# Kernel tuning notes

Hardware: AMD Instinct MI355X
Metric: run time of the kernel (lower is better)

## Reference

```python
import jax, jax.numpy as jnp
import numpy as np

B, N, IN_F, OUT_F = 32, 1024, 256, 256


def setup_inputs() -> dict:
    key = jax.random.key(0)
    k_adj, k_feat, k_w, k_b = jax.random.split(key, 4)
    adjacency = jax.random.uniform(k_adj, (B, N, N), dtype=jnp.float32)  # [B,N,N]
    features = jax.random.normal(k_feat, (B, N, IN_F), dtype=jnp.float32)  # [B,N,in]
    # 'thomas' init ~ uniform(-1/sqrt(fan_in), 1/sqrt(fan_in)) style; scale is
    # irrelevant to correctness-checking, use scaled normal.
    weight = jax.random.normal(k_w, (IN_F, OUT_F), dtype=jnp.float32) / np.sqrt(IN_F)
    bias = jax.random.normal(k_b, (OUT_F,), dtype=jnp.float32) / np.sqrt(IN_F)
    return {"adjacency": adjacency, "features": features, "weight": weight, "bias": bias}


def reference(adjacency, features, weight, bias) -> jnp.ndarray:
    # support = features @ weight : [B,N,out]
    support = jnp.einsum("bni,io->bno", features, weight)
    # output = bmm(adjacency, support) : [B,N,out]
    output = jnp.einsum("bnm,bmo->bno", adjacency, support)
    return output + bias
```

## Files before the change

### kernel.cpp

```cpp
#include <hip/hip_runtime.h>
#include <hip/hip_bf16.h>


typedef __attribute__((__ext_vector_type__(4))) float  f32x4;
typedef __attribute__((__ext_vector_type__(8))) __bf16 bf16x8;
typedef __attribute__((__ext_vector_type__(4))) __bf16 bf16x4;

#define BM  64
#define BN  256
#define BK  32
#define LDP 40

__global__ __launch_bounds__(256) void k_wt(const float* __restrict__ w,
                                            __bf16* __restrict__ Wt) {
  __shared__ __bf16 T[64][65];
  const int bi = blockIdx.x >> 2;
  const int bj = blockIdx.x & 3;
  const int t  = threadIdx.x;
  const int r  = t >> 2;
  const int q  = t & 3;
  const float* src = w + (size_t)(bi * 64 + r) * 256 + bj * 64 + q * 16;
#pragma unroll
  for (int u = 0; u < 4; ++u) {
    f32x4 v = *(const f32x4*)(src + u * 4);
    T[r][q * 16 + u * 4 + 0] = (__bf16)v[0];
    T[r][q * 16 + u * 4 + 1] = (__bf16)v[1];
    T[r][q * 16 + u * 4 + 2] = (__bf16)v[2];
    T[r][q * 16 + u * 4 + 3] = (__bf16)v[3];
  }
  __syncthreads();
  bf16x8 h0, h1;
#pragma unroll
  for (int u = 0; u < 8; ++u) {
    h0[u] = T[q * 16 + u][r];
    h1[u] = T[q * 16 + 8 + u][r];
  }
  __bf16* dst = Wt + (size_t)(bj * 64 + r) * 256 + bi * 64 + q * 16;
  *(bf16x8*)(dst)     = h0;
  *(bf16x8*)(dst + 8) = h1;
}

template <int KTOT, int LDA, int LDB, bool EPI_ST>
__global__ __launch_bounds__(512, 4) void k_gemm(
    const float* __restrict__ Aall, const __bf16* __restrict__ Bg_all,
    const float* __restrict__ bias, float* __restrict__ Out,
    __bf16* __restrict__ St) {
  __shared__ __bf16 As[2][BM * LDP];
  __shared__ __bf16 Bs[2][BN * LDP];

  const int tid  = threadIdx.x;
  const int lane = tid & 63;
  const int wv   = tid >> 6;
  const int wr   = wv >> 2;
  const int wc   = wv & 3;
  const int l16  = lane & 15;
  const int kch  = (lane >> 4) * 8;

  int lg, b, mtile;
  const float*  A;
  const __bf16* Bg;
  if constexpr (EPI_ST) {
    lg    = blockIdx.x;
    b     = lg >> 4;
    mtile = lg & 15;
    A     = Aall + (size_t)lg * BM * LDA;
    Bg    = Bg_all;
  } else {
    const int h = blockIdx.x;
    lg    = (h & 7) * 64 + (h >> 3);
    b     = lg >> 4;
    mtile = lg & 15;
    A     = Aall + (size_t)b * 1024 * 1024 + (size_t)mtile * BM * LDA;
    Bg    = Bg_all + (size_t)b * 256 * 1024;
  }

  const int ar = tid >> 3;
  const int ac = (tid & 7) * 4;
  const int br = tid >> 1;
  const int bh = (tid & 1) * 16;

  const float*  ap = A  + (size_t)ar * LDA + ac;
  const __bf16* bp = Bg + (size_t)br * LDB + bh;

  f32x4  av0, av1;
  bf16x8 bv0[2], bv1[2];

#define LOAD0(k0)                                   \
  av0    = *(const f32x4*)(ap + (k0));              \
  bv0[0] = *(const bf16x8*)(bp + (k0));             \
  bv0[1] = *(const bf16x8*)(bp + (k0) + 8)
#define LOAD1(k0)                                   \
  av1    = *(const f32x4*)(ap + (k0));              \
  bv1[0] = *(const bf16x8*)(bp + (k0));             \
  bv1[1] = *(const bf16x8*)(bp + (k0) + 8)

  auto cvt_write = [&](const f32x4& av, const bf16x8* bv, int buf) {
    bf16x4 h = {(__bf16)av[0], (__bf16)av[1], (__bf16)av[2], (__bf16)av[3]};
    *(bf16x4*)&As[buf][ar * LDP + ac]      = h;
    *(bf16x8*)&Bs[buf][br * LDP + bh]      = bv[0];
    *(bf16x8*)&Bs[buf][br * LDP + bh + 8]  = bv[1];
  };

  f32x4 acc[2][4];
#pragma unroll
  for (int m = 0; m < 2; ++m)
#pragma unroll
    for (int n = 0; n < 4; ++n) acc[m][n] = (f32x4){0.f, 0.f, 0.f, 0.f};

  auto compute = [&](int buf) {
    bf16x8 af[2], bfv[4];
#pragma unroll
    for (int m = 0; m < 2; ++m)
      af[m] = *(const bf16x8*)&As[buf][(wr * 32 + m * 16 + l16) * LDP + kch];
#pragma unroll
    for (int n = 0; n < 4; ++n)
      bfv[n] = *(const bf16x8*)&Bs[buf][(wc * 64 + n * 16 + l16) * LDP + kch];
#pragma unroll
    for (int m = 0; m < 2; ++m)
#pragma unroll
      for (int n = 0; n < 4; ++n)
        acc[m][n] = __builtin_amdgcn_mfma_f32_16x16x32_bf16(af[m], bfv[n], acc[m][n], 0, 0, 0);
  };

  constexpr int NT = KTOT / BK;
  LOAD0(0);
  LOAD1(BK);
  cvt_write(av0, bv0, 0);
  __syncthreads();

  for (int t = 0; t < NT - 2; t += 2) {
    LOAD0((t + 2) * BK);
    compute(0);
    cvt_write(av1, bv1, 1);
    __syncthreads();
    LOAD1((t + 3) * BK);
    compute(1);
    cvt_write(av0, bv0, 0);
    __syncthreads();
  }
  compute(0);
  cvt_write(av1, bv1, 1);
  __syncthreads();
  compute(1);

#undef LOAD0
#undef LOAD1

  const int rg = (lane >> 4) * 4;
  if constexpr (EPI_ST) {
    const int mbase = mtile * BM;
#pragma unroll
    for (int n = 0; n < 4; ++n) {
      const int col = wc * 64 + n * 16 + l16;
      __bf16* dst = St + ((size_t)b * 256 + col) * 1024 + mbase;
#pragma unroll
      for (int m = 0; m < 2; ++m) {
        const int row = wr * 32 + m * 16 + rg;
        bf16x4 hh = {(__bf16)acc[m][n][0], (__bf16)acc[m][n][1],
                     (__bf16)acc[m][n][2], (__bf16)acc[m][n][3]};
        *(bf16x4*)(dst + row) = hh;
      }
    }
  } else {
    float* ob = Out + ((size_t)b * 1024 + (size_t)mtile * BM) * 256;
#pragma unroll
    for (int n = 0; n < 4; ++n) {
      const int col = wc * 64 + n * 16 + l16;
      const float bvs = bias[col];
#pragma unroll
      for (int m = 0; m < 2; ++m) {
        const int row = wr * 32 + m * 16 + rg;
#pragma unroll
        for (int r2 = 0; r2 < 4; ++r2)
          ob[(size_t)(row + r2) * 256 + col] = acc[m][n][r2] + bvs;
      }
    }
  }
}

extern "C" void kernel_launch(void* const* d_in, const int* in_sizes, int n_in,
                              void* d_out, int out_size, void* d_ws, size_t ws_size,
                              hipStream_t stream) {
  const float* adj  = (const float*)d_in[0];
  const float* feat = (const float*)d_in[1];
  const float* w    = (const float*)d_in[2];
  const float* bias = (const float*)d_in[3];
  float* out = (float*)d_out;

  __bf16* Wt = (__bf16*)d_ws;
  __bf16* St = (__bf16*)((char*)d_ws + 131072);

  k_wt<<<16, 256, 0, stream>>>(w, Wt);
  k_gemm<256, 256, 256, true><<<512, 512, 0, stream>>>(feat, Wt, nullptr, nullptr, St);
  k_gemm<1024, 1024, 1024, false><<<512, 512, 0, stream>>>(adj, St, bias, out, nullptr);
}
```

Baseline: 61.68 us.

## Stage GEMM tiles via direct global-to-LDS loads with blocked B layout

Replaces the register-staged load, convert and LDS-write path with global_load_lds direct transfers. A is kept as fp32 in LDS with an XOR swizzle and converted to bf16 at fragment-read time. The intermediate support and transposed weight are stored in a k-blocked [K/8][N][8] layout so each B tile is a contiguous chunk. The aim is to cut VGPR use and load/convert instruction overhead, and to let the copy overlap compute. In exchange the fp32 A tile doubles LDS size, and bf16 conversion is repeated per wave when fragments are read.

```diff
diff --git a/kernel.cpp b/kernel.cpp
--- a/kernel.cpp
+++ b/kernel.cpp
@@ -6,10 +6,15 @@
 typedef __attribute__((__ext_vector_type__(8))) __bf16 bf16x8;
 typedef __attribute__((__ext_vector_type__(4))) __bf16 bf16x4;
 
-#define BM  64
-#define BN  256
-#define BK  32
-#define LDP 40
+#define BM 64
+#define BN 256
+#define BK 32
+
+__device__ __forceinline__ void gld16(const void* g, void* l) {
+  __builtin_amdgcn_global_load_lds(
+      (const __attribute__((address_space(1))) unsigned int*)g,
+      (__attribute__((address_space(3))) unsigned int*)l, 16, 0, 0);
+}
 
 __global__ __launch_bounds__(256) void k_wt(const float* __restrict__ w,
                                             __bf16* __restrict__ Wt) {
@@ -35,70 +40,54 @@
     h0[u] = T[q * 16 + u][r];
     h1[u] = T[q * 16 + 8 + u][r];
   }
-  __bf16* dst = Wt + (size_t)(bj * 64 + r) * 256 + bi * 64 + q * 16;
-  *(bf16x8*)(dst)     = h0;
-  *(bf16x8*)(dst + 8) = h1;
+  __bf16* d0 = Wt + ((size_t)(bi * 8 + q * 2) * 256 + (bj * 64 + r)) * 8;
+  *(bf16x8*)d0          = h0;
+  *(bf16x8*)(d0 + 2048) = h1;
 }
 
-template <int KTOT, int LDA, int LDB, bool EPI_ST>
+template <int KTOT, int LDA, bool EPI_ST>
 __global__ __launch_bounds__(512, 4) void k_gemm(
     const float* __restrict__ Aall, const __bf16* __restrict__ Bg_all,
     const float* __restrict__ bias, float* __restrict__ Out,
     __bf16* __restrict__ St) {
-  __shared__ __bf16 As[2][BM * LDP];
-  __shared__ __bf16 Bs[2][BN * LDP];
+  __shared__ float  Af[2][BM * BK];
+  __shared__ __bf16 Bf[2][4 * BN * 8];
 
   const int tid  = threadIdx.x;
   const int lane = tid & 63;
-  const int wv   = tid >> 6;
-  const int wr   = wv >> 2;
-  const int wc   = wv & 3;
+  const int wid  = tid >> 6;
+  const int wr   = wid >> 2;
+  const int wc   = wid & 3;
   const int l16  = lane & 15;
-  const int kch  = (lane >> 4) * 8;
+  const int g    = lane >> 4;
 
-  int lg, b, mtile;
-  const float*  A;
-  const __bf16* Bg;
+  int b, mtile;
+  const float*  Ablk;
+  const __bf16* Bblk;
   if constexpr (EPI_ST) {
-    lg    = blockIdx.x;
+    const int lg = blockIdx.x;
     b     = lg >> 4;
     mtile = lg & 15;
-    A     = Aall + (size_t)lg * BM * LDA;
-    Bg    = Bg_all;
+    Ablk  = Aall + (size_t)lg * BM * LDA;
+    Bblk  = Bg_all;
   } else {
-    const int h = blockIdx.x;
-    lg    = (h & 7) * 64 + (h >> 3);
+    const int h  = blockIdx.x;
+    const int lg = (h & 7) * 64 + (h >> 3);
     b     = lg >> 4;
     mtile = lg & 15;
-    A     = Aall + (size_t)b * 1024 * 1024 + (size_t)mtile * BM * LDA;
-    Bg    = Bg_all + (size_t)b * 256 * 1024;
+    Ablk  = Aall + (size_t)b * 1024 * 1024 + (size_t)mtile * BM * LDA;
+    Bblk  = Bg_all + (size_t)b * 262144;
   }
 
-  const int ar = tid >> 3;
-  const int ac = (tid & 7) * 4;
-  const int br = tid >> 1;
-  const int bh = (tid & 1) * 16;
+  const int    ar   = tid >> 3;
+  const float* asrc = Ablk + (size_t)ar * LDA + (((tid & 7) ^ (ar & 7)) << 2);
+  const __bf16* bs0 = Bblk + ((size_t)wid * 128 + lane) * 8;
 
-  const float*  ap = A  + (size_t)ar * LDA + ac;
-  const __bf16* bp = Bg + (size_t)br * LDB + bh;
-
-  f32x4  av0, av1;
-  bf16x8 bv0[2], bv1[2];
-
-#define LOAD0(k0)                                   \
-  av0    = *(const f32x4*)(ap + (k0));              \
-  bv0[0] = *(const bf16x8*)(bp + (k0));             \
-  bv0[1] = *(const bf16x8*)(bp + (k0) + 8)
-#define LOAD1(k0)                                   \
-  av1    = *(const f32x4*)(ap + (k0));              \
-  bv1[0] = *(const bf16x8*)(bp + (k0));             \
-  bv1[1] = *(const bf16x8*)(bp + (k0) + 8)
-
-  auto cvt_write = [&](const f32x4& av, const bf16x8* bv, int buf) {
-    bf16x4 h = {(__bf16)av[0], (__bf16)av[1], (__bf16)av[2], (__bf16)av[3]};
-    *(bf16x4*)&As[buf][ar * LDP + ac]      = h;
-    *(bf16x8*)&Bs[buf][br * LDP + bh]      = bv[0];
-    *(bf16x8*)&Bs[buf][br * LDP + bh + 8]  = bv[1];
+  auto stage = [&](int buf, int k0) {
+    gld16(asrc + k0, &Af[buf][wid * 256]);
+    const __bf16* bt = bs0 + (size_t)(k0 >> 3) * 2048;
+    gld16(bt,       &Bf[buf][wid * 1024]);
+    gld16(bt + 512, &Bf[buf][wid * 1024 + 512]);
   };
 
   f32x4 acc[2][4];
@@ -107,58 +96,56 @@
 #pragma unroll
     for (int n = 0; n < 4; ++n) acc[m][n] = (f32x4){0.f, 0.f, 0.f, 0.f};
 
+  const int h7 = l16 & 7;
   auto compute = [&](int buf) {
-    bf16x8 af[2], bfv[4];
+    bf16x8 af[2], bv[4];
 #pragma unroll
-    for (int m = 0; m < 2; ++m)
-      af[m] = *(const bf16x8*)&As[buf][(wr * 32 + m * 16 + l16) * LDP + kch];
+    for (int m = 0; m < 2; ++m) {
+      const float* base = &Af[buf][(wr * 32 + m * 16 + l16) * BK];
+      f32x4 v0 = *(const f32x4*)(base + (((2 * g)     ^ h7) << 2));
+      f32x4 v1 = *(const f32x4*)(base + (((2 * g + 1) ^ h7) << 2));
+      af[m] = (bf16x8){(__bf16)v0[0], (__bf16)v0[1], (__bf16)v0[2], (__bf16)v0[3],
+                       (__bf16)v1[0], (__bf16)v1[1], (__bf16)v1[2], (__bf16)v1[3]};
+    }
 #pragma unroll
     for (int n = 0; n < 4; ++n)
-      bfv[n] = *(const bf16x8*)&Bs[buf][(wc * 64 + n * 16 + l16) * LDP + kch];
+      bv[n] = *(const bf16x8*)&Bf[buf][(g * 256 + wc * 64 + n * 16 + l16) * 8];
 #pragma unroll
     for (int m = 0; m < 2; ++m)
 #pragma unroll
       for (int n = 0; n < 4; ++n)
-        acc[m][n] = __builtin_amdgcn_mfma_f32_16x16x32_bf16(af[m], bfv[n], acc[m][n], 0, 0, 0);
+        acc[m][n] = __builtin_amdgcn_mfma_f32_16x16x32_bf16(af[m], bv[n], acc[m][n], 0, 0, 0);
   };
 
   constexpr int NT = KTOT / BK;
-  LOAD0(0);
-  LOAD1(BK);
-  cvt_write(av0, bv0, 0);
+  stage(0, 0);
   __syncthreads();
-
   for (int t = 0; t < NT - 2; t += 2) {
-    LOAD0((t + 2) * BK);
+    stage(1, (t + 1) * BK);
     compute(0);
-    cvt_write(av1, bv1, 1);
     __syncthreads();
-    LOAD1((t + 3) * BK);
+    stage(0, (t + 2) * BK);
     compute(1);
-    cvt_write(av0, bv0, 0);
     __syncthreads();
   }
+  stage(1, (NT - 1) * BK);
   compute(0);
-  cvt_write(av1, bv1, 1);
   __syncthreads();
   compute(1);
 
-#undef LOAD0
-#undef LOAD1
-
   const int rg = (lane >> 4) * 4;
   if constexpr (EPI_ST) {
-    const int mbase = mtile * BM;
+    __bf16* Stb = St + (size_t)b * 262144;
 #pragma unroll
     for (int n = 0; n < 4; ++n) {
       const int col = wc * 64 + n * 16 + l16;
-      __bf16* dst = St + ((size_t)b * 256 + col) * 1024 + mbase;
 #pragma unroll
       for (int m = 0; m < 2; ++m) {
-        const int row = wr * 32 + m * 16 + rg;
+        const int gm = mtile * 64 + wr * 32 + m * 16 + rg;
+        __bf16* dst = Stb + ((size_t)(gm >> 3) * 256 + col) * 8 + (gm & 7);
         bf16x4 hh = {(__bf16)acc[m][n][0], (__bf16)acc[m][n][1],
                      (__bf16)acc[m][n][2], (__bf16)acc[m][n][3]};
-        *(bf16x4*)(dst + row) = hh;
+        *(bf16x4*)dst = hh;
       }
     }
   } else {
@@ -191,6 +178,6 @@
   __bf16* St = (__bf16*)((char*)d_ws + 131072);
 
   k_wt<<<16, 256, 0, stream>>>(w, Wt);
-  k_gemm<256, 256, 256, true><<<512, 512, 0, stream>>>(feat, Wt, nullptr, nullptr, St);
-  k_gemm<1024, 1024, 1024, false><<<512, 512, 0, stream>>>(adj, St, bias, out, nullptr);
+  k_gemm<256, 256, true><<<512, 512, 0, stream>>>(feat, Wt, nullptr, nullptr, St);
+  k_gemm<1024, 1024, false><<<512, 512, 0, stream>>>(adj, St, bias, out, nullptr);
 }
```

Result: faster. 54.37 us (-11.8%).
